# Performance work log

Hardware: AMD Instinct MI355X
Metric: run time of the kernel (lower is better)

## Reference

```python
import jax, jax.numpy as jnp
import numpy as np

B, T = 64, 512
N_EMB, HIDDEN, VOCAB = 768, 256, 3072


def setup_inputs() -> dict:
    key = jax.random.key(0)
    ks = jax.random.split(key, 5)
    def xavier(k, shape):
        bound = float(np.sqrt(6.0 / (shape[0] + shape[1])))
        return jax.random.uniform(k, shape, jnp.float32, -bound, bound)
    return {
        "idx": jax.random.randint(ks[0], (B, T), 0, VOCAB),
        "emb_table": jax.random.normal(ks[1], (VOCAB, N_EMB), jnp.float32),
        "Wxh": xavier(ks[2], (N_EMB, HIDDEN)),
        "Whh": xavier(ks[3], (HIDDEN, HIDDEN)),
        "Wy": xavier(ks[4], (HIDDEN, VOCAB)),
        "By": jnp.zeros((VOCAB,), jnp.float32),
        "Bh": jnp.zeros((HIDDEN,), jnp.float32),
    }


def reference(idx, emb_table, Wxh, Whh, Wy, By, Bh):
    # embedded: [B, T, E] -> scan over time with hidden carry [B, H]
    embedded = emb_table[idx]                      # gather
    xWxh = jnp.einsum('bte,eh->tbh', embedded, Wxh)  # precompute input projection

    def step(hidden, x_t):
        hidden = jnp.tanh(x_t + hidden @ Whh + Bh)
        return hidden, None

    h0 = jnp.zeros((idx.shape[0], Whh.shape[0]), embedded.dtype)
    hidden, _ = jax.lax.scan(step, h0, xWxh)
    # return_sequences=False: only the last step's output is returned
    out = hidden @ Wy + By
    return out, hidden
```

## Files before the change

### kernel.cpp

```cpp
#include <hip/hip_runtime.h>
#include <hip/hip_bf16.h>

typedef _Float16 half8 __attribute__((ext_vector_type(8)));
typedef float f32x4 __attribute__((ext_vector_type(4)));

#define B_SZ 64
#define T_SZ 512
#define E_SZ 768
#define H_SZ 256
#define V_SZ 3072

#define WS_X     0u
#define WS_WT    16777216u
#define WS_WF    17170432u
#define WS_H     17301504u

static __device__ __forceinline__ float fast_tanh(float x) {
  float e = __builtin_amdgcn_exp2f(x * 2.8853900817779268f);
  return 1.0f - 2.0f * __builtin_amdgcn_rcpf(1.0f + e);
}

__global__ __launch_bounds__(256) void k0_convert(
    const float* __restrict__ Wxh,
    const float* __restrict__ Whh,
    _Float16* __restrict__ Wt,
    _Float16* __restrict__ Wf)
{
  int gid = blockIdx.x * 256 + threadIdx.x;
  if (gid < E_SZ * H_SZ) {
    int e = gid >> 8, h = gid & 255;
    Wt[h * E_SZ + e] = (_Float16)Wxh[gid];
  }
  if (gid < 65536) {
    int j = gid & 7, lane = (gid >> 3) & 63, kt = (gid >> 9) & 7, nt = gid >> 12;
    int quad = lane >> 4, n16 = lane & 15;
    int row = kt * 32 + quad * 8 + j, col = nt * 16 + n16;
    Wf[gid] = (_Float16)Whh[row * H_SZ + col];
  }
}

__global__ __launch_bounds__(256) void k1_xproj(
    const int* __restrict__ idx,
    const float* __restrict__ emb,
    const _Float16* __restrict__ Wt,
    _Float16* __restrict__ x)
{
  const int tid  = threadIdx.x;
  const int w    = tid >> 6;
  const int lane = tid & 63;
  const int m16  = lane & 15;
  const int quad = lane >> 4;
  const int r = blockIdx.x * 64 + w * 16 + m16;
  const int t = r >> 6;
  const int b = r & 63;
  const int erow = idx[b * T_SZ + t];
  const float* Arow = emb + (size_t)erow * E_SZ + quad * 8;

  __shared__ __align__(16) _Float16 bp[2][16 * 64 * 8];
  int n_[4], kb_[4];
#pragma unroll
  for (int pp = 0; pp < 4; ++pp) {
    int f = tid + 256 * pp;
    n_[pp]  = ((f >> 6) << 4) | (f & 15);
    kb_[pp] = (f >> 4) & 3;
  }
  uint4 stg[4];
#pragma unroll
  for (int pp = 0; pp < 4; ++pp)
    stg[pp] = *(const uint4*)(Wt + (size_t)n_[pp] * E_SZ + kb_[pp] * 8);
  f32x4 af0 = *(const f32x4*)(Arow);
  f32x4 af1 = *(const f32x4*)(Arow + 4);

  f32x4 acc[16];
#pragma unroll
  for (int n = 0; n < 16; ++n) { f32x4 z = {0.f, 0.f, 0.f, 0.f}; acc[n] = z; }

#pragma unroll
  for (int pp = 0; pp < 4; ++pp)
    *(uint4*)(bp[0] + (size_t)(tid + 256 * pp) * 8) = stg[pp];
  __syncthreads();

#pragma unroll 1
  for (int ki = 0; ki < 24; ++ki) {
    const _Float16* cur = bp[ki & 1];
    f32x4 af0n = af0, af1n = af1;
    if (ki < 23) {
#pragma unroll
      for (int pp = 0; pp < 4; ++pp)
        stg[pp] = *(const uint4*)(Wt + (size_t)n_[pp] * E_SZ + (ki + 1) * 32 + kb_[pp] * 8);
      af0n = *(const f32x4*)(Arow + (ki + 1) * 32);
      af1n = *(const f32x4*)(Arow + (ki + 1) * 32 + 4);
    }
    half8 a;
#pragma unroll
    for (int e = 0; e < 4; ++e) { a[e] = (_Float16)af0[e]; a[4 + e] = (_Float16)af1[e]; }
#pragma unroll
    for (int nt = 0; nt < 16; ++nt) {
      half8 bb = *(const half8*)(cur + (size_t)(nt * 64 + lane) * 8);
      acc[nt] = __builtin_amdgcn_mfma_f32_16x16x32_f16(a, bb, acc[nt], 0, 0, 0);
    }
    if (ki < 23) {
#pragma unroll
      for (int pp = 0; pp < 4; ++pp)
        *(uint4*)(bp[(ki + 1) & 1] + (size_t)(tid + 256 * pp) * 8) = stg[pp];
      __syncthreads();
    }
    af0 = af0n; af1 = af1n;
  }
  const int rbase = blockIdx.x * 64 + w * 16 + quad * 4;
#pragma unroll
  for (int nt = 0; nt < 16; ++nt) {
    const int col = nt * 16 + m16;
#pragma unroll
    for (int rg = 0; rg < 4; ++rg) {
      x[(size_t)(rbase + rg) * H_SZ + col] = (_Float16)acc[nt][rg];
    }
  }
}

#define LDFRAG(C, KT, R0, R1, R2, R3) { \
  uint4 q = Wf4[(((size_t)(w * 4 + C) * 8 + KT) * 64) + lane]; \
  asm volatile("v_accvgpr_write_b32 a" #R0 ", %0" :: "v"(q.x) : "a" #R0); \
  asm volatile("v_accvgpr_write_b32 a" #R1 ", %0" :: "v"(q.y) : "a" #R1); \
  asm volatile("v_accvgpr_write_b32 a" #R2 ", %0" :: "v"(q.z) : "a" #R2); \
  asm volatile("v_accvgpr_write_b32 a" #R3 ", %0" :: "v"(q.w) : "a" #R3); }

#define MFMA_K0(A0, Z) \
  asm volatile( \
    "v_mfma_f32_16x16x32_f16 %[t0], %[a], a[0:3],   %[z]\n\t" \
    "v_mfma_f32_16x16x32_f16 %[t1], %[a], a[32:35], %[z]\n\t" \
    "v_mfma_f32_16x16x32_f16 %[t2], %[a], a[64:67], %[z]\n\t" \
    "v_mfma_f32_16x16x32_f16 %[t3], %[a], a[96:99], %[z]" \
    : [t0] "=&v"(acc0), [t1] "=&v"(acc1), [t2] "=&v"(acc2), [t3] "=&v"(acc3) \
    : [a] "v"(A0), [z] "v"(Z));

#define MFMA_KT(A0, B0, B1, B2, B3) \
  asm volatile( \
    "v_mfma_f32_16x16x32_f16 %[t0], %[a], a[" #B0 "], %[t0]\n\t" \
    "v_mfma_f32_16x16x32_f16 %[t1], %[a], a[" #B1 "], %[t1]\n\t" \
    "v_mfma_f32_16x16x32_f16 %[t2], %[a], a[" #B2 "], %[t2]\n\t" \
    "v_mfma_f32_16x16x32_f16 %[t3], %[a], a[" #B3 "], %[t3]" \
    : [t0] "+v"(acc0), [t1] "+v"(acc1), [t2] "+v"(acc2), [t3] "+v"(acc3) \
    : [a] "v"(A0));

#define MFMA_K7(A0, B0, B1, B2, B3) \
  asm volatile( \
    "v_mfma_f32_16x16x32_f16 %[t0], %[a], a[" #B0 "], %[t0]\n\t" \
    "v_mfma_f32_16x16x32_f16 %[t1], %[a], a[" #B1 "], %[t1]\n\t" \
    "v_mfma_f32_16x16x32_f16 %[t2], %[a], a[" #B2 "], %[t2]\n\t" \
    "v_mfma_f32_16x16x32_f16 %[t3], %[a], a[" #B3 "], %[t3]\n\t" \
    "s_nop 7\n\t" \
    "s_nop 7" \
    : [t0] "+v"(acc0), [t1] "+v"(acc1), [t2] "+v"(acc2), [t3] "+v"(acc3) \
    : [a] "v"(A0));

__global__ __launch_bounds__(256) void k2_rnn(
    const _Float16* __restrict__ Wf,
    const _Float16* __restrict__ x,
    const float* __restrict__ Bh,
    float* __restrict__ hout,
    float* __restrict__ hidout)
{
  const int b    = blockIdx.x;
  const int tid  = threadIdx.x;
  const int w    = tid >> 6;
  const int lane = tid & 63;
  const int quad = lane >> 4;
  __shared__ __align__(16) _Float16 hb[2][H_SZ];
  const uint4* Wf4 = (const uint4*)Wf;

  LDFRAG(0,0,  0,  1,  2,  3)  LDFRAG(0,1,  4,  5,  6,  7)
  LDFRAG(0,2,  8,  9, 10, 11)  LDFRAG(0,3, 12, 13, 14, 15)
  LDFRAG(0,4, 16, 17, 18, 19)  LDFRAG(0,5, 20, 21, 22, 23)
  LDFRAG(0,6, 24, 25, 26, 27)  LDFRAG(0,7, 28, 29, 30, 31)
  LDFRAG(1,0, 32, 33, 34, 35)  LDFRAG(1,1, 36, 37, 38, 39)
  LDFRAG(1,2, 40, 41, 42, 43)  LDFRAG(1,3, 44, 45, 46, 47)
  LDFRAG(1,4, 48, 49, 50, 51)  LDFRAG(1,5, 52, 53, 54, 55)
  LDFRAG(1,6, 56, 57, 58, 59)  LDFRAG(1,7, 60, 61, 62, 63)
  LDFRAG(2,0, 64, 65, 66, 67)  LDFRAG(2,1, 68, 69, 70, 71)
  LDFRAG(2,2, 72, 73, 74, 75)  LDFRAG(2,3, 76, 77, 78, 79)
  LDFRAG(2,4, 80, 81, 82, 83)  LDFRAG(2,5, 84, 85, 86, 87)
  LDFRAG(2,6, 88, 89, 90, 91)  LDFRAG(2,7, 92, 93, 94, 95)
  LDFRAG(3,0, 96, 97, 98, 99)  LDFRAG(3,1,100,101,102,103)
  LDFRAG(3,2,104,105,106,107)  LDFRAG(3,3,108,109,110,111)
  LDFRAG(3,4,112,113,114,115)  LDFRAG(3,5,116,117,118,119)
  LDFRAG(3,6,120,121,122,123)  LDFRAG(3,7,124,125,126,127)

  const float bhj = Bh[tid];
  const _Float16* xp = x + b * H_SZ + tid;
  _Float16 xq = xp[0];
  f32x4 zero4 = {0.f, 0.f, 0.f, 0.f};
  asm volatile("" : "+v"(zero4));
  hb[1][tid] = (_Float16)0.f;
  float hval = 0.f;
  __syncthreads();

#pragma unroll 1
  for (int t = 0; t < T_SZ; ++t) {
    const int tn = (t < T_SZ - 1) ? (t + 1) : t;
    _Float16 xn = xp[(size_t)tn * (B_SZ * H_SZ)];
    const _Float16* hr = hb[(t + 1) & 1];
    half8 va0 = *(const half8*)(hr +   0 + quad * 8);
    half8 va1 = *(const half8*)(hr +  32 + quad * 8);
    half8 va2 = *(const half8*)(hr +  64 + quad * 8);
    half8 va3 = *(const half8*)(hr +  96 + quad * 8);
    half8 va4 = *(const half8*)(hr + 128 + quad * 8);
    half8 va5 = *(const half8*)(hr + 160 + quad * 8);
    half8 va6 = *(const half8*)(hr + 192 + quad * 8);
    half8 va7 = *(const half8*)(hr + 224 + quad * 8);
    f32x4 acc0, acc1, acc2, acc3;
    MFMA_K0(va0, zero4)
    MFMA_KT(va1,   4:7,  36:39,  68:71, 100:103)
    MFMA_KT(va2,  8:11,  40:43,  72:75, 104:107)
    MFMA_KT(va3, 12:15,  44:47,  76:79, 108:111)
    MFMA_KT(va4, 16:19,  48:51,  80:83, 112:115)
    MFMA_KT(va5, 20:23,  52:55,  84:87, 116:119)
    MFMA_KT(va6, 24:27,  56:59,  88:91, 120:123)
    MFMA_K7(va7, 28:31,  60:63,  92:95, 124:127)
    float v0 = acc0[0], v1 = acc1[0], v2 = acc2[0], v3 = acc3[0];
    float ylo = (quad & 1) ? v1 : v0;
    float yhi = (quad & 1) ? v3 : v2;
    float y   = (quad & 2) ? yhi : ylo;
    hval = fast_tanh(y + (float)xq + bhj);
    hb[t & 1][tid] = (_Float16)hval;
    __syncthreads();
    xq = xn;
  }
  hout[b * H_SZ + tid] = hval;
  hidout[b * H_SZ + tid] = hval;
}

__global__ __launch_bounds__(256) void k3_out(
    const float* __restrict__ h,
    const float* __restrict__ Wy,
    const float* __restrict__ By,
    float* __restrict__ out)
{
  __shared__ float hs[H_SZ];
  const int c = blockIdx.x;
  const int b = blockIdx.y;
  const int v = c * 256 + threadIdx.x;
  hs[threadIdx.x] = h[b * H_SZ + threadIdx.x];
  __syncthreads();
  float acc = By[v];
#pragma unroll 8
  for (int jj = 0; jj < H_SZ; ++jj) {
    acc += hs[jj] * Wy[(size_t)jj * V_SZ + v];
  }
  out[(size_t)b * V_SZ + v] = acc;
}

extern "C" void kernel_launch(void* const* d_in, const int* in_sizes, int n_in,
                              void* d_out, int out_size, void* d_ws, size_t ws_size,
                              hipStream_t stream)
{
  const int*   idx = (const int*)d_in[0];
  const float* emb = (const float*)d_in[1];
  const float* Wxh = (const float*)d_in[2];
  const float* Whh = (const float*)d_in[3];
  const float* Wy  = (const float*)d_in[4];
  const float* By  = (const float*)d_in[5];
  const float* Bh  = (const float*)d_in[6];

  char* ws = (char*)d_ws;
  _Float16* x    = (_Float16*)(ws + WS_X);
  _Float16* Wt   = (_Float16*)(ws + WS_WT);
  _Float16* Wf   = (_Float16*)(ws + WS_WF);
  float*    hbuf = (float*)(ws + WS_H);

  float* out    = (float*)d_out;
  float* hidout = out + (size_t)B_SZ * V_SZ;

  k0_convert<<<768, 256, 0, stream>>>(Wxh, Whh, Wt, Wf);
  k1_xproj  <<<512, 256, 0, stream>>>(idx, emb, Wt, x);
  k2_rnn    <<<64, 256, 0, stream>>>(Wf, x, Bh, hbuf, hidout);
  k3_out    <<<dim3(12, 64), 256, 0, stream>>>(hbuf, Wy, By, out);
}
```

Before: 387.4 us.

## Replace MFMA recurrence with per-thread fp16 dot2 over register-resident Whh column

The recurrent step no longer uses MFMA with Whh fragments in AGPRs. Each thread now holds its own column of Whh as 128 packed half2 registers, loaded and converted directly from fp32, and computes its hidden unit with v_dot2 instructions over the hidden vector broadcast from LDS. The time loop is unrolled by two with static ping-pong buffers, and the Wf conversion pass is removed from k0. The aim is to cut MFMA latency and the lane-select overhead on the serial critical path. The cost is 128 dot2 ops per step per thread plus 32 broadcast LDS reads, and high VGPR pressure.

```diff
diff --git a/kernel.cpp b/kernel.cpp
--- a/kernel.cpp
+++ b/kernel.cpp
@@ -2,6 +2,7 @@
 #include <hip/hip_bf16.h>
 
 typedef _Float16 half8 __attribute__((ext_vector_type(8)));
+typedef _Float16 half2_t __attribute__((ext_vector_type(2)));
 typedef float f32x4 __attribute__((ext_vector_type(4)));
 
 #define B_SZ 64
@@ -20,22 +21,19 @@
   return 1.0f - 2.0f * __builtin_amdgcn_rcpf(1.0f + e);
 }
 
+static __device__ __forceinline__ float dot2(unsigned int h2, unsigned int w2, float c) {
+  return __builtin_amdgcn_fdot2(__builtin_bit_cast(half2_t, h2),
+                                __builtin_bit_cast(half2_t, w2), c, false);
+}
+
 __global__ __launch_bounds__(256) void k0_convert(
     const float* __restrict__ Wxh,
-    const float* __restrict__ Whh,
-    _Float16* __restrict__ Wt,
-    _Float16* __restrict__ Wf)
+    _Float16* __restrict__ Wt)
 {
   int gid = blockIdx.x * 256 + threadIdx.x;
   if (gid < E_SZ * H_SZ) {
     int e = gid >> 8, h = gid & 255;
     Wt[h * E_SZ + e] = (_Float16)Wxh[gid];
-  }
-  if (gid < 65536) {
-    int j = gid & 7, lane = (gid >> 3) & 63, kt = (gid >> 9) & 7, nt = gid >> 12;
-    int quad = lane >> 4, n16 = lane & 15;
-    int row = kt * 32 + quad * 8 + j, col = nt * 16 + n16;
-    Wf[gid] = (_Float16)Whh[row * H_SZ + col];
   }
 }
 
@@ -118,114 +116,64 @@
   }
 }
 
-#define LDFRAG(C, KT, R0, R1, R2, R3) { \
-  uint4 q = Wf4[(((size_t)(w * 4 + C) * 8 + KT) * 64) + lane]; \
-  asm volatile("v_accvgpr_write_b32 a" #R0 ", %0" :: "v"(q.x) : "a" #R0); \
-  asm volatile("v_accvgpr_write_b32 a" #R1 ", %0" :: "v"(q.y) : "a" #R1); \
-  asm volatile("v_accvgpr_write_b32 a" #R2 ", %0" :: "v"(q.z) : "a" #R2); \
-  asm volatile("v_accvgpr_write_b32 a" #R3 ", %0" :: "v"(q.w) : "a" #R3); }
-
-#define MFMA_K0(A0, Z) \
-  asm volatile( \
-    "v_mfma_f32_16x16x32_f16 %[t0], %[a], a[0:3],   %[z]\n\t" \
-    "v_mfma_f32_16x16x32_f16 %[t1], %[a], a[32:35], %[z]\n\t" \
-    "v_mfma_f32_16x16x32_f16 %[t2], %[a], a[64:67], %[z]\n\t" \
-    "v_mfma_f32_16x16x32_f16 %[t3], %[a], a[96:99], %[z]" \
-    : [t0] "=&v"(acc0), [t1] "=&v"(acc1), [t2] "=&v"(acc2), [t3] "=&v"(acc3) \
-    : [a] "v"(A0), [z] "v"(Z));
-
-#define MFMA_KT(A0, B0, B1, B2, B3) \
-  asm volatile( \
-    "v_mfma_f32_16x16x32_f16 %[t0], %[a], a[" #B0 "], %[t0]\n\t" \
-    "v_mfma_f32_16x16x32_f16 %[t1], %[a], a[" #B1 "], %[t1]\n\t" \
-    "v_mfma_f32_16x16x32_f16 %[t2], %[a], a[" #B2 "], %[t2]\n\t" \
-    "v_mfma_f32_16x16x32_f16 %[t3], %[a], a[" #B3 "], %[t3]" \
-    : [t0] "+v"(acc0), [t1] "+v"(acc1), [t2] "+v"(acc2), [t3] "+v"(acc3) \
-    : [a] "v"(A0));
-
-#define MFMA_K7(A0, B0, B1, B2, B3) \
-  asm volatile( \
-    "v_mfma_f32_16x16x32_f16 %[t0], %[a], a[" #B0 "], %[t0]\n\t" \
-    "v_mfma_f32_16x16x32_f16 %[t1], %[a], a[" #B1 "], %[t1]\n\t" \
-    "v_mfma_f32_16x16x32_f16 %[t2], %[a], a[" #B2 "], %[t2]\n\t" \
-    "v_mfma_f32_16x16x32_f16 %[t3], %[a], a[" #B3 "], %[t3]\n\t" \
-    "s_nop 7\n\t" \
-    "s_nop 7" \
-    : [t0] "+v"(acc0), [t1] "+v"(acc1), [t2] "+v"(acc2), [t3] "+v"(acc3) \
-    : [a] "v"(A0));
-
-__global__ __launch_bounds__(256) void k2_rnn(
-    const _Float16* __restrict__ Wf,
+__global__ __launch_bounds__(256, 1) void k2_rnn(
+    const float* __restrict__ Whh,
     const _Float16* __restrict__ x,
     const float* __restrict__ Bh,
     float* __restrict__ hout,
     float* __restrict__ hidout)
 {
-  const int b    = blockIdx.x;
-  const int tid  = threadIdx.x;
-  const int w    = tid >> 6;
-  const int lane = tid & 63;
-  const int quad = lane >> 4;
+  const int b   = blockIdx.x;
+  const int tid = threadIdx.x;
   __shared__ __align__(16) _Float16 hb[2][H_SZ];
-  const uint4* Wf4 = (const uint4*)Wf;
-
-  LDFRAG(0,0,  0,  1,  2,  3)  LDFRAG(0,1,  4,  5,  6,  7)
-  LDFRAG(0,2,  8,  9, 10, 11)  LDFRAG(0,3, 12, 13, 14, 15)
-  LDFRAG(0,4, 16, 17, 18, 19)  LDFRAG(0,5, 20, 21, 22, 23)
-  LDFRAG(0,6, 24, 25, 26, 27)  LDFRAG(0,7, 28, 29, 30, 31)
-  LDFRAG(1,0, 32, 33, 34, 35)  LDFRAG(1,1, 36, 37, 38, 39)
-  LDFRAG(1,2, 40, 41, 42, 43)  LDFRAG(1,3, 44, 45, 46, 47)
-  LDFRAG(1,4, 48, 49, 50, 51)  LDFRAG(1,5, 52, 53, 54, 55)
-  LDFRAG(1,6, 56, 57, 58, 59)  LDFRAG(1,7, 60, 61, 62, 63)
-  LDFRAG(2,0, 64, 65, 66, 67)  LDFRAG(2,1, 68, 69, 70, 71)
-  LDFRAG(2,2, 72, 73, 74, 75)  LDFRAG(2,3, 76, 77, 78, 79)
-  LDFRAG(2,4, 80, 81, 82, 83)  LDFRAG(2,5, 84, 85, 86, 87)
-  LDFRAG(2,6, 88, 89, 90, 91)  LDFRAG(2,7, 92, 93, 94, 95)
-  LDFRAG(3,0, 96, 97, 98, 99)  LDFRAG(3,1,100,101,102,103)
-  LDFRAG(3,2,104,105,106,107)  LDFRAG(3,3,108,109,110,111)
-  LDFRAG(3,4,112,113,114,115)  LDFRAG(3,5,116,117,118,119)
-  LDFRAG(3,6,120,121,122,123)  LDFRAG(3,7,124,125,126,127)
+
+  unsigned int wc[128];
+#pragma unroll
+  for (int p = 0; p < 128; ++p) {
+    _Float16 w0 = (_Float16)Whh[(size_t)(2 * p)     * H_SZ + tid];
+    _Float16 w1 = (_Float16)Whh[(size_t)(2 * p + 1) * H_SZ + tid];
+    half2_t pk; pk[0] = w0; pk[1] = w1;
+    wc[p] = __builtin_bit_cast(unsigned int, pk);
+  }
 
   const float bhj = Bh[tid];
   const _Float16* xp = x + b * H_SZ + tid;
-  _Float16 xq = xp[0];
-  f32x4 zero4 = {0.f, 0.f, 0.f, 0.f};
-  asm volatile("" : "+v"(zero4));
+  _Float16 xA = xp[0];
+  _Float16 xB = xp[(size_t)(B_SZ * H_SZ)];
   hb[1][tid] = (_Float16)0.f;
   float hval = 0.f;
   __syncthreads();
 
+#define RNN_STEP(HR, HW, XF)                                           \
+  {                                                                    \
+    const uint4* hq4 = (const uint4*)(HR);                             \
+    float a0 = 0.f, a1 = 0.f, a2 = 0.f, a3 = 0.f;                      \
+    _Pragma("unroll")                                                  \
+    for (int kk = 0; kk < 32; ++kk) {                                  \
+      uint4 hq = hq4[kk];                                              \
+      a0 = dot2(hq.x, wc[4 * kk + 0], a0);                             \
+      a1 = dot2(hq.y, wc[4 * kk + 1], a1);                             \
+      a2 = dot2(hq.z, wc[4 * kk + 2], a2);                             \
+      a3 = dot2(hq.w, wc[4 * kk + 3], a3);                             \
+    }                                                                  \
+    float y = (a0 + a1) + (a2 + a3);                                   \
+    hval = fast_tanh(y + (XF));                                        \
+    (HW)[tid] = (_Float16)hval;                                        \
+    __syncthreads();                                                   \
+  }
+
 #pragma unroll 1
-  for (int t = 0; t < T_SZ; ++t) {
-    const int tn = (t < T_SZ - 1) ? (t + 1) : t;
-    _Float16 xn = xp[(size_t)tn * (B_SZ * H_SZ)];
-    const _Float16* hr = hb[(t + 1) & 1];
-    half8 va0 = *(const half8*)(hr +   0 + quad * 8);
-    half8 va1 = *(const half8*)(hr +  32 + quad * 8);
-    half8 va2 = *(const half8*)(hr +  64 + quad * 8);
-    half8 va3 = *(const half8*)(hr +  96 + quad * 8);
-    half8 va4 = *(const half8*)(hr + 128 + quad * 8);
-    half8 va5 = *(const half8*)(hr + 160 + quad * 8);
-    half8 va6 = *(const half8*)(hr + 192 + quad * 8);
-    half8 va7 = *(const half8*)(hr + 224 + quad * 8);
-    f32x4 acc0, acc1, acc2, acc3;
-    MFMA_K0(va0, zero4)
-    MFMA_KT(va1,   4:7,  36:39,  68:71, 100:103)
-    MFMA_KT(va2,  8:11,  40:43,  72:75, 104:107)
-    MFMA_KT(va3, 12:15,  44:47,  76:79, 108:111)
-    MFMA_KT(va4, 16:19,  48:51,  80:83, 112:115)
-    MFMA_KT(va5, 20:23,  52:55,  84:87, 116:119)
-    MFMA_KT(va6, 24:27,  56:59,  88:91, 120:123)
-    MFMA_K7(va7, 28:31,  60:63,  92:95, 124:127)
-    float v0 = acc0[0], v1 = acc1[0], v2 = acc2[0], v3 = acc3[0];
-    float ylo = (quad & 1) ? v1 : v0;
-    float yhi = (quad & 1) ? v3 : v2;
-    float y   = (quad & 2) ? yhi : ylo;
-    hval = fast_tanh(y + (float)xq + bhj);
-    hb[t & 1][tid] = (_Float16)hval;
-    __syncthreads();
-    xq = xn;
-  }
+  for (int tt = 0; tt < 256; ++tt) {
+    float xfA = (float)xA + bhj;
+    int ta = 2 * tt + 2; ta = ta > 511 ? 511 : ta;
+    xA = xp[(size_t)ta * (B_SZ * H_SZ)];
+    RNN_STEP(hb[1], hb[0], xfA)
+    float xfB = (float)xB + bhj;
+    int tb = 2 * tt + 3; tb = tb > 511 ? 511 : tb;
+    xB = xp[(size_t)tb * (B_SZ * H_SZ)];
+    RNN_STEP(hb[0], hb[1], xfB)
+  }
+#undef RNN_STEP
   hout[b * H_SZ + tid] = hval;
   hidout[b * H_SZ + tid] = hval;
 }
@@ -265,14 +213,13 @@
   char* ws = (char*)d_ws;
   _Float16* x    = (_Float16*)(ws + WS_X);
   _Float16* Wt   = (_Float16*)(ws + WS_WT);
-  _Float16* Wf   = (_Float16*)(ws + WS_WF);
   float*    hbuf = (float*)(ws + WS_H);
 
   float* out    = (float*)d_out;
   float* hidout = out + (size_t)B_SZ * V_SZ;
 
-  k0_convert<<<768, 256, 0, stream>>>(Wxh, Whh, Wt, Wf);
+  k0_convert<<<768, 256, 0, stream>>>(Wxh, Wt);
   k1_xproj  <<<512, 256, 0, stream>>>(idx, emb, Wt, x);
-  k2_rnn    <<<64, 256, 0, stream>>>(Wf, x, Bh, hbuf, hidout);
+  k2_rnn    <<<64, 256, 0, stream>>>(Whh, x, Bh, hbuf, hidout);
   k3_out    <<<dim3(12, 64), 256, 0, stream>>>(hbuf, Wy, By, out);
 }
```

Measured after the change: 443.6 us. 1.15x slower.

## Batch 16 sequences per RNN block so MFMA uses full N dimension

Applied to the files above, without the earlier changes.

The recurrent kernel now processes 16 batch rows per block instead of one, swapping MFMA operands so the Whh fragments in AGPRs act as A and the 16 hidden states act as B. Each MFMA output lane now holds useful values, and the epilogue writes four tanh results per accumulator into a swizzled LDS tile to avoid bank conflicts. The grid shrinks from 64 blocks to 4, which cuts redundant weight loading and MFMA waste. In exchange, far fewer CUs run the serial 512-step loop, each step does more epilogue and LDS work, and per-step latency may rise.

```diff
diff --git a/kernel.cpp b/kernel.cpp
--- a/kernel.cpp
+++ b/kernel.cpp
@@ -2,6 +2,8 @@
 #include <hip/hip_bf16.h>
 
 typedef _Float16 half8 __attribute__((ext_vector_type(8)));
+typedef _Float16 half4_t __attribute__((ext_vector_type(4)));
+typedef _Float16 half2_t __attribute__((ext_vector_type(2)));
 typedef float f32x4 __attribute__((ext_vector_type(4)));
 
 #define B_SZ 64
@@ -125,48 +127,50 @@
   asm volatile("v_accvgpr_write_b32 a" #R2 ", %0" :: "v"(q.z) : "a" #R2); \
   asm volatile("v_accvgpr_write_b32 a" #R3 ", %0" :: "v"(q.w) : "a" #R3); }
 
-#define MFMA_K0(A0, Z) \
+#define MFMA_K0(B0, Z) \
   asm volatile( \
-    "v_mfma_f32_16x16x32_f16 %[t0], %[a], a[0:3],   %[z]\n\t" \
-    "v_mfma_f32_16x16x32_f16 %[t1], %[a], a[32:35], %[z]\n\t" \
-    "v_mfma_f32_16x16x32_f16 %[t2], %[a], a[64:67], %[z]\n\t" \
-    "v_mfma_f32_16x16x32_f16 %[t3], %[a], a[96:99], %[z]" \
+    "v_mfma_f32_16x16x32_f16 %[t0], a[0:3],   %[b], %[z]\n\t" \
+    "v_mfma_f32_16x16x32_f16 %[t1], a[32:35], %[b], %[z]\n\t" \
+    "v_mfma_f32_16x16x32_f16 %[t2], a[64:67], %[b], %[z]\n\t" \
+    "v_mfma_f32_16x16x32_f16 %[t3], a[96:99], %[b], %[z]" \
     : [t0] "=&v"(acc0), [t1] "=&v"(acc1), [t2] "=&v"(acc2), [t3] "=&v"(acc3) \
-    : [a] "v"(A0), [z] "v"(Z));
-
-#define MFMA_KT(A0, B0, B1, B2, B3) \
+    : [b] "v"(B0), [z] "v"(Z));
+
+#define MFMA_KT(B0, A0, A1, A2, A3) \
   asm volatile( \
-    "v_mfma_f32_16x16x32_f16 %[t0], %[a], a[" #B0 "], %[t0]\n\t" \
-    "v_mfma_f32_16x16x32_f16 %[t1], %[a], a[" #B1 "], %[t1]\n\t" \
-    "v_mfma_f32_16x16x32_f16 %[t2], %[a], a[" #B2 "], %[t2]\n\t" \
-    "v_mfma_f32_16x16x32_f16 %[t3], %[a], a[" #B3 "], %[t3]" \
+    "v_mfma_f32_16x16x32_f16 %[t0], a[" #A0 "], %[b], %[t0]\n\t" \
+    "v_mfma_f32_16x16x32_f16 %[t1], a[" #A1 "], %[b], %[t1]\n\t" \
+    "v_mfma_f32_16x16x32_f16 %[t2], a[" #A2 "], %[b], %[t2]\n\t" \
+    "v_mfma_f32_16x16x32_f16 %[t3], a[" #A3 "], %[b], %[t3]" \
     : [t0] "+v"(acc0), [t1] "+v"(acc1), [t2] "+v"(acc2), [t3] "+v"(acc3) \
-    : [a] "v"(A0));
-
-#define MFMA_K7(A0, B0, B1, B2, B3) \
+    : [b] "v"(B0));
+
+#define MFMA_K7(B0, A0, A1, A2, A3) \
   asm volatile( \
-    "v_mfma_f32_16x16x32_f16 %[t0], %[a], a[" #B0 "], %[t0]\n\t" \
-    "v_mfma_f32_16x16x32_f16 %[t1], %[a], a[" #B1 "], %[t1]\n\t" \
-    "v_mfma_f32_16x16x32_f16 %[t2], %[a], a[" #B2 "], %[t2]\n\t" \
-    "v_mfma_f32_16x16x32_f16 %[t3], %[a], a[" #B3 "], %[t3]\n\t" \
+    "v_mfma_f32_16x16x32_f16 %[t0], a[" #A0 "], %[b], %[t0]\n\t" \
+    "v_mfma_f32_16x16x32_f16 %[t1], a[" #A1 "], %[b], %[t1]\n\t" \
+    "v_mfma_f32_16x16x32_f16 %[t2], a[" #A2 "], %[b], %[t2]\n\t" \
+    "v_mfma_f32_16x16x32_f16 %[t3], a[" #A3 "], %[b], %[t3]\n\t" \
     "s_nop 7\n\t" \
     "s_nop 7" \
     : [t0] "+v"(acc0), [t1] "+v"(acc1), [t2] "+v"(acc2), [t3] "+v"(acc3) \
-    : [a] "v"(A0));
-
-__global__ __launch_bounds__(256) void k2_rnn(
+    : [b] "v"(B0));
+
+__global__ __launch_bounds__(256, 1) void k2_rnn(
     const _Float16* __restrict__ Wf,
     const _Float16* __restrict__ x,
     const float* __restrict__ Bh,
     float* __restrict__ hout,
     float* __restrict__ hidout)
 {
-  const int b    = blockIdx.x;
+  const int blk  = blockIdx.x;
   const int tid  = threadIdx.x;
   const int w    = tid >> 6;
   const int lane = tid & 63;
+  const int m    = lane & 15;
   const int quad = lane >> 4;
-  __shared__ __align__(16) _Float16 hb[2][H_SZ];
+  const int swz  = (m & 7) << 3;
+  __shared__ __align__(16) _Float16 hs[2][16 * H_SZ];
   const uint4* Wf4 = (const uint4*)Wf;
 
   LDFRAG(0,0,  0,  1,  2,  3)  LDFRAG(0,1,  4,  5,  6,  7)
@@ -186,48 +190,89 @@
   LDFRAG(3,4,112,113,114,115)  LDFRAG(3,5,116,117,118,119)
   LDFRAG(3,6,120,121,122,123)  LDFRAG(3,7,124,125,126,127)
 
-  const float bhj = Bh[tid];
-  const _Float16* xp = x + b * H_SZ + tid;
-  _Float16 xq = xp[0];
+  float bhv[16];
+#pragma unroll
+  for (int c = 0; c < 4; ++c)
+#pragma unroll
+    for (int r = 0; r < 4; ++r)
+      bhv[c * 4 + r] = Bh[(w * 4 + c) * 16 + quad * 4 + r];
+
+  const _Float16* xb = x + (size_t)(blk * 16 + m) * H_SZ;
+  uint2 xq0, xq1, xq2, xq3;
+  {
+    const _Float16* xp0 = xb;
+    xq0 = *(const uint2*)(xp0 + (w * 4 + 0) * 16 + quad * 4);
+    xq1 = *(const uint2*)(xp0 + (w * 4 + 1) * 16 + quad * 4);
+    xq2 = *(const uint2*)(xp0 + (w * 4 + 2) * 16 + quad * 4);
+    xq3 = *(const uint2*)(xp0 + (w * 4 + 3) * 16 + quad * 4);
+  }
+
   f32x4 zero4 = {0.f, 0.f, 0.f, 0.f};
   asm volatile("" : "+v"(zero4));
-  hb[1][tid] = (_Float16)0.f;
-  float hval = 0.f;
+#pragma unroll
+  for (int i = 0; i < 16; ++i) hs[1][tid + 256 * i] = (_Float16)0.f;
   __syncthreads();
 
 #pragma unroll 1
   for (int t = 0; t < T_SZ; ++t) {
     const int tn = (t < T_SZ - 1) ? (t + 1) : t;
-    _Float16 xn = xp[(size_t)tn * (B_SZ * H_SZ)];
-    const _Float16* hr = hb[(t + 1) & 1];
-    half8 va0 = *(const half8*)(hr +   0 + quad * 8);
-    half8 va1 = *(const half8*)(hr +  32 + quad * 8);
-    half8 va2 = *(const half8*)(hr +  64 + quad * 8);
-    half8 va3 = *(const half8*)(hr +  96 + quad * 8);
-    half8 va4 = *(const half8*)(hr + 128 + quad * 8);
-    half8 va5 = *(const half8*)(hr + 160 + quad * 8);
-    half8 va6 = *(const half8*)(hr + 192 + quad * 8);
-    half8 va7 = *(const half8*)(hr + 224 + quad * 8);
+    const _Float16* xpn = xb + (size_t)tn * (B_SZ * H_SZ);
+    uint2 xn0 = *(const uint2*)(xpn + (w * 4 + 0) * 16 + quad * 4);
+    uint2 xn1 = *(const uint2*)(xpn + (w * 4 + 1) * 16 + quad * 4);
+    uint2 xn2 = *(const uint2*)(xpn + (w * 4 + 2) * 16 + quad * 4);
+    uint2 xn3 = *(const uint2*)(xpn + (w * 4 + 3) * 16 + quad * 4);
+
+    const _Float16* hr = hs[(t + 1) & 1];
+    _Float16*       hw = hs[t & 1];
+
+    const _Float16* hrm = hr + m * H_SZ;
+    uint4 vb0 = *(const uint4*)(hrm + (( 0 * 32 + quad * 8) ^ swz));
+    uint4 vb1 = *(const uint4*)(hrm + (( 1 * 32 + quad * 8) ^ swz));
+    uint4 vb2 = *(const uint4*)(hrm + (( 2 * 32 + quad * 8) ^ swz));
+    uint4 vb3 = *(const uint4*)(hrm + (( 3 * 32 + quad * 8) ^ swz));
+    uint4 vb4 = *(const uint4*)(hrm + (( 4 * 32 + quad * 8) ^ swz));
+    uint4 vb5 = *(const uint4*)(hrm + (( 5 * 32 + quad * 8) ^ swz));
+    uint4 vb6 = *(const uint4*)(hrm + (( 6 * 32 + quad * 8) ^ swz));
+    uint4 vb7 = *(const uint4*)(hrm + (( 7 * 32 + quad * 8) ^ swz));
+
     f32x4 acc0, acc1, acc2, acc3;
-    MFMA_K0(va0, zero4)
-    MFMA_KT(va1,   4:7,  36:39,  68:71, 100:103)
-    MFMA_KT(va2,  8:11,  40:43,  72:75, 104:107)
-    MFMA_KT(va3, 12:15,  44:47,  76:79, 108:111)
-    MFMA_KT(va4, 16:19,  48:51,  80:83, 112:115)
-    MFMA_KT(va5, 20:23,  52:55,  84:87, 116:119)
-    MFMA_KT(va6, 24:27,  56:59,  88:91, 120:123)
-    MFMA_K7(va7, 28:31,  60:63,  92:95, 124:127)
-    float v0 = acc0[0], v1 = acc1[0], v2 = acc2[0], v3 = acc3[0];
-    float ylo = (quad & 1) ? v1 : v0;
-    float yhi = (quad & 1) ? v3 : v2;
-    float y   = (quad & 2) ? yhi : ylo;
-    hval = fast_tanh(y + (float)xq + bhj);
-    hb[t & 1][tid] = (_Float16)hval;
+    MFMA_K0(__builtin_bit_cast(half8, vb0), zero4)
+    MFMA_KT(__builtin_bit_cast(half8, vb1),   4:7,  36:39,  68:71, 100:103)
+    MFMA_KT(__builtin_bit_cast(half8, vb2),  8:11,  40:43,  72:75, 104:107)
+    MFMA_KT(__builtin_bit_cast(half8, vb3), 12:15,  44:47,  76:79, 108:111)
+    MFMA_KT(__builtin_bit_cast(half8, vb4), 16:19,  48:51,  80:83, 112:115)
+    MFMA_KT(__builtin_bit_cast(half8, vb5), 20:23,  52:55,  84:87, 116:119)
+    MFMA_KT(__builtin_bit_cast(half8, vb6), 24:27,  56:59,  88:91, 120:123)
+    MFMA_K7(__builtin_bit_cast(half8, vb7), 28:31,  60:63,  92:95, 124:127)
+
+#define EPI(C, ACC, XQ) { \
+    half4_t xf = __builtin_bit_cast(half4_t, XQ); \
+    float y0 = fast_tanh(ACC[0] + (float)xf[0] + bhv[C * 4 + 0]); \
+    float y1 = fast_tanh(ACC[1] + (float)xf[1] + bhv[C * 4 + 1]); \
+    float y2 = fast_tanh(ACC[2] + (float)xf[2] + bhv[C * 4 + 2]); \
+    float y3 = fast_tanh(ACC[3] + (float)xf[3] + bhv[C * 4 + 3]); \
+    half2_t plo; plo[0] = (_Float16)y0; plo[1] = (_Float16)y1; \
+    half2_t phi; phi[0] = (_Float16)y2; phi[1] = (_Float16)y3; \
+    uint2 pk; pk.x = __builtin_bit_cast(unsigned int, plo); \
+    pk.y = __builtin_bit_cast(unsigned int, phi); \
+    *(uint2*)(hw + m * H_SZ + ((((w * 4 + C) * 16 + quad * 4)) ^ swz)) = pk; }
+    EPI(0, acc0, xq0)
+    EPI(1, acc1, xq1)
+    EPI(2, acc2, xq2)
+    EPI(3, acc3, xq3)
+#undef EPI
     __syncthreads();
-    xq = xn;
-  }
-  hout[b * H_SZ + tid] = hval;
-  hidout[b * H_SZ + tid] = hval;
+    xq0 = xn0; xq1 = xn1; xq2 = xn2; xq3 = xn3;
+  }
+
+#pragma unroll
+  for (int i = 0; i < 16; ++i) {
+    int idx = tid + 256 * i;
+    int mm = idx >> 8, nn = idx & 255;
+    float v = (float)hs[1][mm * H_SZ + (nn ^ ((mm & 7) << 3))];
+    hout[(size_t)(blk * 16 + mm) * H_SZ + nn]   = v;
+    hidout[(size_t)(blk * 16 + mm) * H_SZ + nn] = v;
+  }
 }
 
 __global__ __launch_bounds__(256) void k3_out(
@@ -273,6 +318,6 @@
 
   k0_convert<<<768, 256, 0, stream>>>(Wxh, Whh, Wt, Wf);
   k1_xproj  <<<512, 256, 0, stream>>>(idx, emb, Wt, x);
-  k2_rnn    <<<64, 256, 0, stream>>>(Wf, x, Bh, hbuf, hidout);
+  k2_rnn    <<<4, 256, 0, stream>>>(Wf, x, Bh, hbuf, hidout);
   k3_out    <<<dim3(12, 64), 256, 0, stream>>>(hbuf, Wy, By, out);
 }
```

Result: slower. 612.0 us (+58.0%).
